# Kernel tuning notes

Measured on AMD Instinct MI355X. Metric: run time of the kernel, lower is better.

The kernel has to match this reference:

```python
import jax, jax.numpy as jnp
import numpy as np
from functools import partial

NUM_INPUTS, NUM_HIDDEN, NUM_OUTPUTS = 2, 10, 4
NUM_STEPS, BATCH = 100, 65536
BETA, THRESHOLD = 0.5, 1.0

# Heaviside spike with ATan surrogate gradient (snntorch default, alpha=2):
# d spk / d u = 1 / (1 + (pi*u)^2)
@jax.custom_vjp
def spike_fn(u):
    return (u > 0.0).astype(u.dtype)

def _spike_fwd(u):
    return spike_fn(u), u

def _spike_bwd(u, g):
    pi = jnp.asarray(np.pi, u.dtype)
    return (g / (1.0 + (pi * u) ** 2),)

spike_fn.defvjp(_spike_fwd, _spike_bwd)

def setup_inputs() -> dict:
    key = jax.random.key(0)
    kx, kw1, kb1, kw2, kb2 = jax.random.split(key, 5)
    x = jax.random.normal(kx, (NUM_STEPS, BATCH, NUM_INPUTS), dtype=jnp.float32)
    # torch.nn.Linear-style init: U(-1/sqrt(fan_in), 1/sqrt(fan_in))
    s1 = 1.0 / np.sqrt(NUM_INPUTS)
    s2 = 1.0 / np.sqrt(NUM_HIDDEN)
    W1 = jax.random.uniform(kw1, (NUM_INPUTS, NUM_HIDDEN), jnp.float32, -s1, s1)
    b1 = jax.random.uniform(kb1, (NUM_HIDDEN,), jnp.float32, -s1, s1)
    W2 = jax.random.uniform(kw2, (NUM_HIDDEN, NUM_OUTPUTS), jnp.float32, -s2, s2)
    b2 = jax.random.uniform(kb2, (NUM_OUTPUTS,), jnp.float32, -s2, s2)
    return {"x": x, "W1": W1, "b1": b1, "W2": W2, "b2": b2}

def _snn_forward(x, W1, b1, W2, b2):
    B = x.shape[1]
    mem1_0 = jnp.zeros((B, NUM_HIDDEN), x.dtype)
    mem2_0 = jnp.zeros((B, NUM_OUTPUTS), x.dtype)
    spk1_0 = jnp.zeros((B, NUM_HIDDEN), x.dtype)
    spk2_0 = jnp.zeros((B, NUM_OUTPUTS), x.dtype)

    def step(carry, x_t):
        mem1, mem2, spk1_prev, spk2_prev = carry
        curr1 = x_t @ W1 + b1  # [B, H]
        # snntorch Leaky, reset_mechanism='subtract': reset uses previous spike
        mem1 = BETA * mem1 + curr1 - spk1_prev * THRESHOLD
        spk1 = spike_fn(mem1 - THRESHOLD)
        curr2 = spk1 @ W2 + b2  # [B, O]
        mem2 = BETA * mem2 + curr2 - spk2_prev * THRESHOLD
        spk2 = spike_fn(mem2 - THRESHOLD)
        return (mem1, mem2, spk1, spk2), (spk1, mem1, spk2, mem2)

    _, (spk1_rec, mem1_rec, spk2_rec, mem2_rec) = jax.lax.scan(
        step, (mem1_0, mem2_0, spk1_0, spk2_0), x)
    return spk1_rec, mem1_rec, spk2_rec, mem2_rec

@jax.jit
def reference(x, W1, b1, W2, b2):
    return _snn_forward(x, W1, b1, W2, b2)
```

## Files before the change

### kernel.cpp

```cpp
#include <hip/hip_runtime.h>


#define T_STEPS 100
#define BATCH   65536
#define NI      2
#define NH      10
#define NO      4
#define LPAD    14

__global__ __launch_bounds__(256) void snn_fwd_kernel(
    const float* __restrict__ x,
    const float* __restrict__ W1,
    const float* __restrict__ b1,
    const float* __restrict__ W2,
    const float* __restrict__ b2,
    float* __restrict__ out)
{
    __shared__ float lds[2][4][64][LPAD];

    const int tid  = threadIdx.x;
    const int lane = tid & 63;
    const int wv   = tid >> 6;
    const int b    = blockIdx.x * 256 + tid;
    const int wb0  = blockIdx.x * 256 + wv * 64;

    float w1[NI][NH], bb1[NH], w2[NH][NO], bb2[NO];
#pragma unroll
    for (int i = 0; i < NI; ++i)
#pragma unroll
        for (int h = 0; h < NH; ++h) w1[i][h] = W1[i * NH + h];
#pragma unroll
    for (int h = 0; h < NH; ++h) bb1[h] = b1[h];
#pragma unroll
    for (int h = 0; h < NH; ++h)
#pragma unroll
        for (int o = 0; o < NO; ++o) w2[h][o] = W2[h * NO + o];
#pragma unroll
    for (int o = 0; o < NO; ++o) bb2[o] = b2[o];

    float mem1[NH], spk1[NH], mem2[NO], spk2[NO];
#pragma unroll
    for (int h = 0; h < NH; ++h) { mem1[h] = 0.0f; spk1[h] = 0.0f; }
#pragma unroll
    for (int o = 0; o < NO; ++o) { mem2[o] = 0.0f; spk2[o] = 0.0f; }

    const size_t O_MEM1 = (size_t)T_STEPS * BATCH * NH;
    const size_t O_SPK2 = 2 * O_MEM1;
    const size_t O_MEM2 = O_SPK2 + (size_t)T_STEPS * BATCH * NO;

    float* p_s1 = out + (size_t)wb0 * NH;
    float* p_m1 = out + O_MEM1 + (size_t)wb0 * NH;
    float* p_s2 = out + O_SPK2 + (size_t)b * NO;
    float* p_m2 = out + O_MEM2 + (size_t)b * NO;
    const size_t stride1 = (size_t)BATCH * NH;
    const size_t stride2 = (size_t)BATCH * NO;

    int q[5], lw[5];
#pragma unroll
    for (int k = 0; k < 5; ++k) {
        const int qq = k * 128 + 2 * lane;
        q[k]  = qq;
        lw[k] = (qq / 10) * LPAD + (qq % 10);
    }
    const float* lsl0 = &lds[0][wv][0][0];
    const float* lsl1 = &lds[1][wv][0][0];

    const float2* x2 = (const float2*)x;
    float2 xv = x2[b];
    float2 xn = x2[(size_t)BATCH + b];

    for (int t = 0; t < T_STEPS; ++t) {
        const size_t pf = (t + 2 < T_STEPS) ? (size_t)(t + 2) * BATCH + b : (size_t)b;
        float2 xn2 = x2[pf];

        float s1new[NH];
#pragma unroll
        for (int h = 0; h < NH; ++h) {
            float c = xv.x * w1[0][h] + xv.y * w1[1][h] + bb1[h];
            float m = 0.5f * mem1[h] + c - spk1[h];
            mem1[h] = m;
            s1new[h] = (m > 1.0f) ? 1.0f : 0.0f;
        }

        float c2[NO];
#pragma unroll
        for (int o = 0; o < NO; ++o) c2[o] = 0.0f;
#pragma unroll
        for (int h = 0; h < NH; ++h)
#pragma unroll
            for (int o = 0; o < NO; ++o)
                c2[o] += s1new[h] * w2[h][o];

        float s2new[NO];
#pragma unroll
        for (int o = 0; o < NO; ++o) {
            float c = c2[o] + bb2[o];
            float m = 0.5f * mem2[o] + c - spk2[o];
            mem2[o] = m;
            s2new[o] = (m > 1.0f) ? 1.0f : 0.0f;
        }

#pragma unroll
        for (int h = 0; h < NH; h += 2) {
            *(float2*)&lds[0][wv][lane][h] = make_float2(s1new[h], s1new[h + 1]);
            *(float2*)&lds[1][wv][lane][h] = make_float2(mem1[h], mem1[h + 1]);
        }
#pragma unroll
        for (int k = 0; k < 5; ++k) {
            const float2 v0 = *(const float2*)(lsl0 + lw[k]);
            const float2 v1 = *(const float2*)(lsl1 + lw[k]);
            *(float2*)(p_s1 + q[k]) = v0;
            *(float2*)(p_m1 + q[k]) = v1;
        }

        *(float4*)p_s2 = make_float4(s2new[0], s2new[1], s2new[2], s2new[3]);
        *(float4*)p_m2 = make_float4(mem2[0], mem2[1], mem2[2], mem2[3]);

#pragma unroll
        for (int h = 0; h < NH; ++h) spk1[h] = s1new[h];
#pragma unroll
        for (int o = 0; o < NO; ++o) spk2[o] = s2new[o];

        p_s1 += stride1; p_m1 += stride1;
        p_s2 += stride2; p_m2 += stride2;
        xv = xn; xn = xn2;
    }
}

extern "C" void kernel_launch(void* const* d_in, const int* in_sizes, int n_in,
                              void* d_out, int out_size, void* d_ws, size_t ws_size,
                              hipStream_t stream) {
    const float* x  = (const float*)d_in[0];
    const float* W1 = (const float*)d_in[1];
    const float* b1 = (const float*)d_in[2];
    const float* W2 = (const float*)d_in[3];
    const float* b2 = (const float*)d_in[4];
    float* out = (float*)d_out;

    dim3 block(256);
    dim3 grid(BATCH / 256);
    snn_fwd_kernel<<<grid, block, 0, stream>>>(x, W1, b1, W2, b2, out);
}
```

Baseline: 787.5 us.

## Split each batch row across two lanes and double-buffer LDS transposes

Each batch element is now handled by a pair of lanes, each owning five hidden neurons, with spikes exchanged by a lane shuffle so both lanes can compute the output layer. One lane writes spk2 and the other writes mem2. The grid doubles to expose more parallelism and store throughput. LDS staging for the hidden-layer outputs is double-buffered, so the global stores for step t-1 are issued after step t is computed. The output-layer matmul is now done redundantly in both lanes, and correctness depends on lockstep wavefront execution within the shared LDS buffers, since there is no barrier.

Result: no change. 786.3 us (-0.1%).

```diff
diff --git a/kernel.cpp b/kernel.cpp
--- a/kernel.cpp
+++ b/kernel.cpp
@@ -3,10 +3,8 @@
 
 #define T_STEPS 100
 #define BATCH   65536
-#define NI      2
 #define NH      10
 #define NO      4
-#define LPAD    14
 
 __global__ __launch_bounds__(256) void snn_fwd_kernel(
     const float* __restrict__ x,
@@ -16,21 +14,26 @@
     const float* __restrict__ b2,
     float* __restrict__ out)
 {
-    __shared__ float lds[2][4][64][LPAD];
+    __shared__ float lds[2][2][4][320];
 
     const int tid  = threadIdx.x;
     const int lane = tid & 63;
     const int wv   = tid >> 6;
-    const int b    = blockIdx.x * 256 + tid;
-    const int wb0  = blockIdx.x * 256 + wv * 64;
+    const int s    = lane & 1;
+    const int gtid = blockIdx.x * 256 + tid;
+    const int p    = gtid >> 1;
+    const int wp0  = blockIdx.x * 128 + wv * 32;
 
-    float w1[NI][NH], bb1[NH], w2[NH][NO], bb2[NO];
+    const int h0 = 5 * s;
+    float w1[2][5], bb1[5];
 #pragma unroll
-    for (int i = 0; i < NI; ++i)
+    for (int i = 0; i < 2; ++i)
 #pragma unroll
-        for (int h = 0; h < NH; ++h) w1[i][h] = W1[i * NH + h];
+        for (int j = 0; j < 5; ++j) w1[i][j] = W1[i * NH + h0 + j];
 #pragma unroll
-    for (int h = 0; h < NH; ++h) bb1[h] = b1[h];
+    for (int j = 0; j < 5; ++j) bb1[j] = b1[h0 + j];
+
+    float w2[NH][NO], bb2[NO];
 #pragma unroll
     for (int h = 0; h < NH; ++h)
 #pragma unroll
@@ -38,50 +41,45 @@
 #pragma unroll
     for (int o = 0; o < NO; ++o) bb2[o] = b2[o];
 
-    float mem1[NH], spk1[NH], mem2[NO], spk2[NO];
+    float mem1[5], spk1[5], mem2[NO], spk2[NO];
 #pragma unroll
-    for (int h = 0; h < NH; ++h) { mem1[h] = 0.0f; spk1[h] = 0.0f; }
+    for (int j = 0; j < 5; ++j) { mem1[j] = 0.0f; spk1[j] = 0.0f; }
 #pragma unroll
     for (int o = 0; o < NO; ++o) { mem2[o] = 0.0f; spk2[o] = 0.0f; }
 
     const size_t O_MEM1 = (size_t)T_STEPS * BATCH * NH;
     const size_t O_SPK2 = 2 * O_MEM1;
     const size_t O_MEM2 = O_SPK2 + (size_t)T_STEPS * BATCH * NO;
-
-    float* p_s1 = out + (size_t)wb0 * NH;
-    float* p_m1 = out + O_MEM1 + (size_t)wb0 * NH;
-    float* p_s2 = out + O_SPK2 + (size_t)b * NO;
-    float* p_m2 = out + O_MEM2 + (size_t)b * NO;
     const size_t stride1 = (size_t)BATCH * NH;
     const size_t stride2 = (size_t)BATCH * NO;
 
-    int q[5], lw[5];
-#pragma unroll
-    for (int k = 0; k < 5; ++k) {
-        const int qq = k * 128 + 2 * lane;
-        q[k]  = qq;
-        lw[k] = (qq / 10) * LPAD + (qq % 10);
-    }
-    const float* lsl0 = &lds[0][wv][0][0];
-    const float* lsl1 = &lds[1][wv][0][0];
+    float* p_s1  = out + (size_t)wp0 * NH;
+    float* p_m1  = out + O_MEM1 + (size_t)wp0 * NH;
+    float* p_sm2 = out + (s ? O_MEM2 : O_SPK2) + (size_t)p * NO;
 
     const float2* x2 = (const float2*)x;
-    float2 xv = x2[b];
-    float2 xn = x2[(size_t)BATCH + b];
+    float2 xv = x2[p];
+    float2 xa = x2[(size_t)BATCH + p];
+    float2 xb = x2[2 * (size_t)BATCH + p];
 
-    for (int t = 0; t < T_STEPS; ++t) {
-        const size_t pf = (t + 2 < T_STEPS) ? (size_t)(t + 2) * BATCH + b : (size_t)b;
-        float2 xn2 = x2[pf];
-
-        float s1new[NH];
+    auto compute_step = [&](float2 xin, float* s1new) {
 #pragma unroll
-        for (int h = 0; h < NH; ++h) {
-            float c = xv.x * w1[0][h] + xv.y * w1[1][h] + bb1[h];
-            float m = 0.5f * mem1[h] + c - spk1[h];
-            mem1[h] = m;
-            s1new[h] = (m > 1.0f) ? 1.0f : 0.0f;
+        for (int j = 0; j < 5; ++j) {
+            float c = xin.x * w1[0][j] + xin.y * w1[1][j] + bb1[j];
+            float m = 0.5f * mem1[j] + c - spk1[j];
+            mem1[j] = m;
+            s1new[j] = (m > 1.0f) ? 1.0f : 0.0f;
+            spk1[j]  = s1new[j];
         }
-
+        float oth[5];
+#pragma unroll
+        for (int j = 0; j < 5; ++j) oth[j] = __shfl_xor(s1new[j], 1);
+        float s1all[10];
+#pragma unroll
+        for (int j = 0; j < 5; ++j) {
+            s1all[j]     = s ? oth[j]   : s1new[j];
+            s1all[5 + j] = s ? s1new[j] : oth[j];
+        }
         float c2[NO];
 #pragma unroll
         for (int o = 0; o < NO; ++o) c2[o] = 0.0f;
@@ -89,41 +87,77 @@
         for (int h = 0; h < NH; ++h)
 #pragma unroll
             for (int o = 0; o < NO; ++o)
-                c2[o] += s1new[h] * w2[h][o];
-
-        float s2new[NO];
+                c2[o] = fmaf(s1all[h], w2[h][o], c2[o]);
+        float4 v2;
+        float s2new[NO], m2v[NO];
 #pragma unroll
         for (int o = 0; o < NO; ++o) {
             float c = c2[o] + bb2[o];
             float m = 0.5f * mem2[o] + c - spk2[o];
-            mem2[o] = m;
+            mem2[o] = m; m2v[o] = m;
             s2new[o] = (m > 1.0f) ? 1.0f : 0.0f;
+            spk2[o]  = s2new[o];
+        }
+        v2.x = s ? m2v[0] : s2new[0];
+        v2.y = s ? m2v[1] : s2new[1];
+        v2.z = s ? m2v[2] : s2new[2];
+        v2.w = s ? m2v[3] : s2new[3];
+        *(float4*)p_sm2 = v2;
+        p_sm2 += stride2;
+    };
+
+    {
+        float s1new[5];
+        compute_step(xv, s1new);
+        float* wr0 = &lds[0][0][wv][0];
+        float* wr1 = &lds[0][1][wv][0];
+#pragma unroll
+        for (int j = 0; j < 5; ++j) {
+            wr0[5 * lane + j] = s1new[j];
+            wr1[5 * lane + j] = mem1[j];
+        }
+        xv = xa; xa = xb;
+    }
+
+    for (int t = 1; t < T_STEPS; ++t) {
+        const int bt = t & 1;
+        const size_t pf = (t + 2 < T_STEPS) ? ((size_t)(t + 2) * BATCH + p) : (size_t)p;
+        xb = x2[pf];
+
+        const float* rd0 = &lds[bt ^ 1][0][wv][0];
+        const float* rd1 = &lds[bt ^ 1][1][wv][0];
+        const float4 a0 = *(const float4*)(rd0 + 4 * lane);
+        const float  a1 = rd0[256 + lane];
+        const float4 b0 = *(const float4*)(rd1 + 4 * lane);
+        const float  b1v = rd1[256 + lane];
+
+        float s1new[5];
+        compute_step(xv, s1new);
+
+        float* wr0 = &lds[bt][0][wv][0];
+        float* wr1 = &lds[bt][1][wv][0];
+#pragma unroll
+        for (int j = 0; j < 5; ++j) {
+            wr0[5 * lane + j] = s1new[j];
+            wr1[5 * lane + j] = mem1[j];
         }
 
-#pragma unroll
-        for (int h = 0; h < NH; h += 2) {
-            *(float2*)&lds[0][wv][lane][h] = make_float2(s1new[h], s1new[h + 1]);
-            *(float2*)&lds[1][wv][lane][h] = make_float2(mem1[h], mem1[h + 1]);
-        }
-#pragma unroll
-        for (int k = 0; k < 5; ++k) {
-            const float2 v0 = *(const float2*)(lsl0 + lw[k]);
-            const float2 v1 = *(const float2*)(lsl1 + lw[k]);
-            *(float2*)(p_s1 + q[k]) = v0;
-            *(float2*)(p_m1 + q[k]) = v1;
-        }
+        *(float4*)(p_s1 + 4 * lane) = a0;
+        p_s1[256 + lane]            = a1;
+        *(float4*)(p_m1 + 4 * lane) = b0;
+        p_m1[256 + lane]            = b1v;
+        p_s1 += stride1; p_m1 += stride1;
 
-        *(float4*)p_s2 = make_float4(s2new[0], s2new[1], s2new[2], s2new[3]);
-        *(float4*)p_m2 = make_float4(mem2[0], mem2[1], mem2[2], mem2[3]);
+        xv = xa; xa = xb;
+    }
 
-#pragma unroll
-        for (int h = 0; h < NH; ++h) spk1[h] = s1new[h];
-#pragma unroll
-        for (int o = 0; o < NO; ++o) spk2[o] = s2new[o];
-
-        p_s1 += stride1; p_m1 += stride1;
-        p_s2 += stride2; p_m2 += stride2;
-        xv = xn; xn = xn2;
+    {
+        const float* rd0 = &lds[(T_STEPS - 1) & 1][0][wv][0];
+        const float* rd1 = &lds[(T_STEPS - 1) & 1][1][wv][0];
+        *(float4*)(p_s1 + 4 * lane) = *(const float4*)(rd0 + 4 * lane);
+        p_s1[256 + lane]            = rd0[256 + lane];
+        *(float4*)(p_m1 + 4 * lane) = *(const float4*)(rd1 + 4 * lane);
+        p_m1[256 + lane]            = rd1[256 + lane];
     }
 }
 
@@ -138,6 +172,6 @@
     float* out = (float*)d_out;
 
     dim3 block(256);
-    dim3 grid(BATCH / 256);
+    dim3 grid((BATCH * 2) / 256);
     snn_fwd_kernel<<<grid, block, 0, stream>>>(x, W1, b1, W2, b2, out);
 }
```
